# Kernel optimization log

Hardware: AMD Instinct MI355X
Metric: run time of the kernel (lower is better)

## Reference

```python
import jax, jax.numpy as jnp
import numpy as np

# angular momenta of the full basis (2s,3s,2p,3p,3d) -> block sizes 1,1,3,3,5; norb=13
L_LIST = [0, 0, 1, 1, 2]


def factor_matrix():
    """Replicates the orbital-pair loop: factor 0.5 on diagonal orbital blocks,
    1.0 for i<j blocks, 0.0 below the block diagonal (only i<=j filled)."""
    sizes = [2 * l + 1 for l in L_LIST]
    norb = sum(sizes)
    F = np.zeros((norb, norb), np.float32)
    ist = 0
    for i, si in enumerate(sizes):
        jst = 0
        for j, sj in enumerate(sizes):
            if i < j:
                F[ist:ist + si, jst:jst + sj] = 1.0
            elif i == j:
                F[ist:ist + si, jst:jst + sj] = 0.5
            jst += sj
        ist += si
    return jnp.asarray(F)


def setup_inputs() -> dict:
    key = jax.random.key(0)
    k1, k2, k3, k4, k5 = jax.random.split(key, 5)
    N, E, K = 128, 2048, 16
    norb = sum(2 * l + 1 for l in L_LIST)  # 13
    return {
        "hopping": jax.random.normal(k1, (E, norb * norb), jnp.float32),
        "onsite": jax.random.normal(k2, (N, norb * norb), jnp.float32),
        "kpoints": jax.random.uniform(k3, (K, 3), jnp.float32),
        "cell_shift": jax.random.normal(k4, (E, 3), jnp.float32),
        "edge_index": jax.random.randint(k5, (2, E), 0, N, jnp.int64),
    }


def reference(hopping, onsite, kpoints, cell_shift, edge_index):
    F = factor_matrix()
    norb = F.shape[0]
    N = onsite.shape[0]
    K = kpoints.shape[0]
    ctype = jnp.complex64

    # per-edge / per-atom orbital blocks with upper-triangular factor (i<=j loop)
    hop = (hopping.reshape(-1, norb, norb) * F).astype(ctype)   # [E,norb,norb]
    ons = (onsite.reshape(-1, norb, norb) * F).astype(ctype)    # [N,norb,norb]

    # Bloch phase exp(-i 2*pi k.R) per (k, edge)
    phase = jnp.exp(-1j * 2.0 * jnp.pi * (kpoints @ cell_shift.T).astype(ctype))  # [K,E]

    # assemble block Hamiltonian [K, N, N, norb, norb]
    H = jnp.zeros((K, N, N, norb, norb), ctype)
    ar = jnp.arange(N)
    H = H.at[:, ar, ar].add(ons[None])  # onsite diagonal blocks (no phase)
    ie, je = edge_index[0], edge_index[1]
    H = H.at[:, ie, je].add(phase[:, :, None, None] * hop[None])  # scatter-add edges

    # hermitize: block + block^H (swap atom blocks and orbital indices)
    H = H + jnp.conj(jnp.swapaxes(jnp.swapaxes(H, 1, 2), 3, 4))
    # [K, N, norb, N, norb] -> [K, all_norb, all_norb]
    Hk = H.transpose(0, 1, 3, 2, 4).reshape(K, N * norb, N * norb)
    return Hk
```

## Files before the change

kernel.cpp:

```cpp
#include <hip/hip_runtime.h>
#include <math.h>

#define NORB 13
#define NORB2 (NORB * NORB)
#define GB 16
#define KSPLIT 2
#define MAXE 128
#define NTHR 256

typedef float fx2 __attribute__((ext_vector_type(2)));

__device__ __forceinline__ int blk_of(int p) {
    return p < 1 ? 0 : (p < 2 ? 1 : (p < 5 ? 2 : (p < 8 ? 3 : 4)));
}
__device__ __forceinline__ float ffac(int p, int q) {
    int bp = blk_of(p), bq = blk_of(q);
    return bp < bq ? 1.0f : (bp == bq ? 0.5f : 0.0f);
}

__global__ void __launch_bounds__(NTHR)
k_fused(const float* __restrict__ hopping,
        const float* __restrict__ onsite,
        const float* __restrict__ kpoints,
        const float* __restrict__ cell_shift,
        const int* __restrict__ edge_index,
        float* __restrict__ out,
        int N, int E, int K, int ld, int es, int ngroups) {
    int g  = blockIdx.x % ngroups;
    int a  = (blockIdx.x / ngroups) % N;
    int kc = blockIdx.x / (ngroups * N);
    int kch = (K + KSPLIT - 1) / KSPLIT;
    int k0 = kc * kch, k1 = min(K, k0 + kch);
    int tid = threadIdx.x;
    int b0 = g * GB;

    __shared__ int cnt[GB + 1];
    __shared__ int cur[GB];
    __shared__ int list[MAXE];

    if (tid <= GB) cnt[tid] = 0;
    __syncthreads();

    for (int e = tid; e < E; e += NTHR) {
        int ie = edge_index[e], je = edge_index[E + e];
        if (ie == a && (je >> 4) == g) atomicAdd(&cnt[je & 15], 1);
        if (je == a && (ie >> 4) == g) atomicAdd(&cnt[ie & 15], 1);
    }
    __syncthreads();
    if (tid == 0) {
        int run = 0;
        for (int i = 0; i < GB; ++i) { int c = cnt[i]; cnt[i] = run; cur[i] = run; run += c; }
        cnt[GB] = run;
    }
    __syncthreads();
    for (int e = tid; e < E; e += NTHR) {
        int ie = edge_index[e], je = edge_index[E + e];
        if (ie == a && (je >> 4) == g) {
            int pos = atomicAdd(&cur[je & 15], 1);
            if (pos < MAXE) list[pos] = (e << 1);
        }
        if (je == a && (ie >> 4) == g) {
            int pos = atomicAdd(&cur[ie & 15], 1);
            if (pos < MAXE) list[pos] = (e << 1) | 1;
        }
    }
    __syncthreads();

    int offs[GB + 1];
    #pragma unroll
    for (int i = 0; i <= GB; ++i) offs[i] = __builtin_amdgcn_readfirstlane(cnt[i]);

    if (tid >= NORB2) return;
    int p = tid / NORB, q = tid - p * NORB;
    float fpq = ffac(p, q), fqp = ffac(q, p);
    int idxF = p * NORB + q, idxR = q * NORB + p;

    bool dwg = (a >= b0) && (a < b0 + GB);
    int idiag = a - b0;
    float onx = 0.f;
    if (dwg) {
        const float* on = onsite + (size_t)a * NORB2;
        onx = on[idxF] * fpq + on[idxR] * fqp;
    }

    for (int k = k0; k < k1; ++k) {
        float kx = kpoints[3 * k], ky = kpoints[3 * k + 1], kz = kpoints[3 * k + 2];
        size_t rowc = ((size_t)(k * ld + a * NORB + p)) * ld + (size_t)b0 * NORB + q;

        #pragma unroll
        for (int i = 0; i < GB; ++i) {
            float ax = (dwg && i == idiag) ? onx : 0.f;
            float ay = 0.f;
            int itend = offs[i + 1];
            for (int it = offs[i]; it < itend; ++it) {
                int ent = __builtin_amdgcn_readfirstlane(list[it]);
                int e = ent >> 1;
                const float* cs = cell_shift + 3 * (size_t)e;
                float d = kx * cs[0] + ky * cs[1] + kz * cs[2];
                float s, c;
                __sincosf(-6.2831853071795864f * d, &s, &c);
                const float* h = hopping + (size_t)e * NORB2;
                float hv, im;
                if (ent & 1) { hv = h[idxR] * fqp; im = -s; }
                else         { hv = h[idxF] * fpq; im =  s; }
                ax += c * hv;
                ay += im * hv;
            }
            if (b0 + i < N) {
                if (es == 2) {
                    fx2* o2 = (fx2*)out;
                    o2[rowc + (size_t)i * NORB] = (fx2){ax, ay};
                } else {
                    out[rowc + (size_t)i * NORB] = ax;
                }
            }
        }
    }
}

extern "C" void kernel_launch(void* const* d_in, const int* in_sizes, int n_in,
                              void* d_out, int out_size, void* d_ws, size_t ws_size,
                              hipStream_t stream) {
    const float* hopping    = (const float*)d_in[0];
    const float* onsite     = (const float*)d_in[1];
    const float* kpoints    = (const float*)d_in[2];
    const float* cell_shift = (const float*)d_in[3];
    const int*   edge_index = (const int*)d_in[4];
    float* out = (float*)d_out;

    int E = in_sizes[0] / NORB2;
    int N = in_sizes[1] / NORB2;
    int K = in_sizes[2] / 3;
    int ld = N * NORB;
    int ngroups = (N + GB - 1) / GB;

    size_t full = (size_t)K * ld * ld * 2;
    int es = ((size_t)out_size >= full) ? 2 : 1;

    int nwg = N * ngroups * KSPLIT;
    k_fused<<<nwg, NTHR, 0, stream>>>(hopping, onsite, kpoints, cell_shift,
                                      edge_index, out, N, E, K, ld, es, ngroups);
}
```

Measured before the change: 213.0 us.

## Remap threads to output columns and use a single unsorted edge list

```diff
diff --git a/kernel.cpp b/kernel.cpp
--- a/kernel.cpp
+++ b/kernel.cpp
@@ -4,6 +4,7 @@
 #define NORB 13
 #define NORB2 (NORB * NORB)
 #define GB 16
+#define NCOL (GB * NORB)
 #define KSPLIT 2
 #define MAXE 128
 #define NTHR 256
@@ -13,8 +14,7 @@
 __device__ __forceinline__ int blk_of(int p) {
     return p < 1 ? 0 : (p < 2 ? 1 : (p < 5 ? 2 : (p < 8 ? 3 : 4)));
 }
-__device__ __forceinline__ float ffac(int p, int q) {
-    int bp = blk_of(p), bq = blk_of(q);
+__device__ __forceinline__ float bfac(int bp, int bq) {
     return bp < bq ? 1.0f : (bp == bq ? 0.5f : 0.0f);
 }
 
@@ -34,86 +34,90 @@
     int tid = threadIdx.x;
     int b0 = g * GB;
 
-    __shared__ int cnt[GB + 1];
-    __shared__ int cur[GB];
+    __shared__ int ecnt;
     __shared__ int list[MAXE];
 
-    if (tid <= GB) cnt[tid] = 0;
+    if (tid == 0) ecnt = 0;
     __syncthreads();
 
     for (int e = tid; e < E; e += NTHR) {
         int ie = edge_index[e], je = edge_index[E + e];
-        if (ie == a && (je >> 4) == g) atomicAdd(&cnt[je & 15], 1);
-        if (je == a && (ie >> 4) == g) atomicAdd(&cnt[ie & 15], 1);
-    }
-    __syncthreads();
-    if (tid == 0) {
-        int run = 0;
-        for (int i = 0; i < GB; ++i) { int c = cnt[i]; cnt[i] = run; cur[i] = run; run += c; }
-        cnt[GB] = run;
-    }
-    __syncthreads();
-    for (int e = tid; e < E; e += NTHR) {
-        int ie = edge_index[e], je = edge_index[E + e];
         if (ie == a && (je >> 4) == g) {
-            int pos = atomicAdd(&cur[je & 15], 1);
-            if (pos < MAXE) list[pos] = (e << 1);
+            int pos = atomicAdd(&ecnt, 1);
+            if (pos < MAXE) list[pos] = (e << 5) | ((je & 15) << 1);
         }
         if (je == a && (ie >> 4) == g) {
-            int pos = atomicAdd(&cur[ie & 15], 1);
-            if (pos < MAXE) list[pos] = (e << 1) | 1;
+            int pos = atomicAdd(&ecnt, 1);
+            if (pos < MAXE) list[pos] = (e << 5) | ((ie & 15) << 1) | 1;
         }
     }
     __syncthreads();
+    int nent = min(__builtin_amdgcn_readfirstlane(ecnt), MAXE);
 
-    int offs[GB + 1];
-    #pragma unroll
-    for (int i = 0; i <= GB; ++i) offs[i] = __builtin_amdgcn_readfirstlane(cnt[i]);
+    int lane = tid & 63;
+    int myent = (lane < nent) ? list[lane] : 0;
 
-    if (tid >= NORB2) return;
-    int p = tid / NORB, q = tid - p * NORB;
-    float fpq = ffac(p, q), fqp = ffac(q, p);
-    int idxF = p * NORB + q, idxR = q * NORB + p;
-
-    bool dwg = (a >= b0) && (a < b0 + GB);
-    int idiag = a - b0;
-    float onx = 0.f;
-    if (dwg) {
-        const float* on = onsite + (size_t)a * NORB2;
-        onx = on[idxF] * fpq + on[idxR] * fqp;
-    }
+    int c = tid;
+    if (c >= NCOL || g * NCOL + c >= ld) return;
+    int i_c = c / NORB;
+    int q   = c - i_c * NORB;
+    int bq  = blk_of(q);
+    bool diagact = (b0 + i_c == a);
+    const float* on = onsite + (size_t)a * NORB2;
 
     for (int k = k0; k < k1; ++k) {
         float kx = kpoints[3 * k], ky = kpoints[3 * k + 1], kz = kpoints[3 * k + 2];
-        size_t rowc = ((size_t)(k * ld + a * NORB + p)) * ld + (size_t)b0 * NORB + q;
 
+        float ax[NORB], ay[NORB];
         #pragma unroll
-        for (int i = 0; i < GB; ++i) {
-            float ax = (dwg && i == idiag) ? onx : 0.f;
-            float ay = 0.f;
-            int itend = offs[i + 1];
-            for (int it = offs[i]; it < itend; ++it) {
-                int ent = __builtin_amdgcn_readfirstlane(list[it]);
-                int e = ent >> 1;
-                const float* cs = cell_shift + 3 * (size_t)e;
-                float d = kx * cs[0] + ky * cs[1] + kz * cs[2];
-                float s, c;
-                __sincosf(-6.2831853071795864f * d, &s, &c);
+        for (int p = 0; p < NORB; ++p) {
+            float v = 0.f;
+            if (diagact) {
+                int bp = blk_of(p);
+                v = on[p * NORB + q] * bfac(bp, bq)
+                  + on[q * NORB + p] * bfac(bq, bp);
+            }
+            ax[p] = v; ay[p] = 0.f;
+        }
+
+        for (int it = 0; it < nent; ++it) {
+            int ent = (it < 64) ? __builtin_amdgcn_readlane(myent, it) : list[it];
+            int e = ent >> 5;
+            int islot = (ent >> 1) & 15;
+            int rev = ent & 1;
+            const float* cs = cell_shift + 3 * (size_t)e;
+            float d = kx * cs[0] + ky * cs[1] + kz * cs[2];
+            float s, cc;
+            __sincosf(-6.2831853071795864f * d, &s, &cc);
+            float sv = rev ? -s : s;
+            if (i_c == islot) {
                 const float* h = hopping + (size_t)e * NORB2;
-                float hv, im;
-                if (ent & 1) { hv = h[idxR] * fqp; im = -s; }
-                else         { hv = h[idxF] * fpq; im =  s; }
-                ax += c * hv;
-                ay += im * hv;
-            }
-            if (b0 + i < N) {
-                if (es == 2) {
-                    fx2* o2 = (fx2*)out;
-                    o2[rowc + (size_t)i * NORB] = (fx2){ax, ay};
+                if (rev) {
+                    #pragma unroll
+                    for (int p = 0; p < NORB; ++p) {
+                        float hv = h[q * NORB + p] * bfac(bq, blk_of(p));
+                        ax[p] += cc * hv; ay[p] += sv * hv;
+                    }
                 } else {
-                    out[rowc + (size_t)i * NORB] = ax;
+                    #pragma unroll
+                    for (int p = 0; p < NORB; ++p) {
+                        float hv = h[p * NORB + q] * bfac(blk_of(p), bq);
+                        ax[p] += cc * hv; ay[p] += sv * hv;
+                    }
                 }
             }
+        }
+
+        size_t base = ((size_t)(k * ld + a * NORB)) * ld + (size_t)g * NCOL + c;
+        if (es == 2) {
+            fx2* o2 = (fx2*)out;
+            #pragma unroll
+            for (int p = 0; p < NORB; ++p)
+                o2[base + (size_t)p * ld] = (fx2){ax[p], ay[p]};
+        } else {
+            #pragma unroll
+            for (int p = 0; p < NORB; ++p)
+                out[base + (size_t)p * ld] = ax[p];
         }
     }
 }
```

Result: faster. 207.9 us (-2.4%).
